# Kernel tuning notes

Measured on AMD Instinct MI355X. Metric: run time of the kernel, lower is better.

## Reference

```python
import jax, jax.numpy as jnp
import numpy as np

N_NODES = 2176
N_IN = 64
N_HID = 2048
N_OUT = 64
NODE_DIM = 64
HEADS = 4


def _build_edge_index():
    hs, os_ = N_IN, N_IN + N_HID
    # input -> hidden block (order: for i: for h)
    s1 = np.repeat(np.arange(0, N_IN), N_HID)
    t1 = np.tile(np.arange(hs, os_), N_IN)
    # hidden -> output block (order: for h: for o)
    s2 = np.repeat(np.arange(hs, os_), N_OUT)
    t2 = np.tile(np.arange(os_, N_NODES), N_HID)
    return jnp.asarray(np.stack([np.concatenate([s1, s2]), np.concatenate([t1, t2])]), dtype=jnp.int32)


def setup_inputs() -> dict:
    key = jax.random.key(0)
    ks = jax.random.split(key, 20)
    D, H = NODE_DIM, HEADS
    edge_index = _build_edge_index()  # [2, E]
    E = edge_index.shape[1]

    def xavier(k, shape):
        fan_in, fan_out = shape[0], shape[1]
        lim = float(np.sqrt(6.0 / (fan_in + fan_out)))
        return jax.random.uniform(k, shape, jnp.float32, -lim, lim)

    return {
        "x_input": jax.random.normal(ks[0], (N_IN,), jnp.float32),
        "node_features": jax.random.normal(ks[1], (N_NODES, D), jnp.float32) * 0.1,
        "edge_weights": jax.random.normal(ks[2], (E, 1), jnp.float32) * 0.1,
        "edge_index": edge_index,
        "wq1": xavier(ks[3], (D, D * H)), "wk1": xavier(ks[4], (D, D * H)),
        "wv1": xavier(ks[5], (D, D * H)), "we1": xavier(ks[6], (1, H)),
        "wo1": xavier(ks[7], (D * H, D)), "bo1": jnp.zeros((D,), jnp.float32),
        "wq2": xavier(ks[8], (D, D * H)), "wk2": xavier(ks[9], (D, D * H)),
        "wv2": xavier(ks[10], (D, D * H)), "we2": xavier(ks[11], (1, H)),
        "wo2": xavier(ks[12], (D * H, D)), "bo2": jnp.zeros((D,), jnp.float32),
        "wproj": xavier(ks[13], (D, 1)), "bproj": jnp.zeros((1,), jnp.float32),
        "num_output_nodes": N_OUT,
    }


def _message_pass(x, edge_index, ew, wq, wk, wv, we, wo, bo):
    # x: [N, D_in]; edge_index: [2, E]; ew: [E, 1]
    src, tgt = edge_index[0], edge_index[1]
    dout = wo.shape[1]
    heads = wq.shape[1] // dout
    q = (x[tgt] @ wq).reshape(-1, heads, dout)  # [E, H, D]
    k = (x[src] @ wk).reshape(-1, heads, dout)
    v = (x[src] @ wv).reshape(-1, heads, dout)
    attn = (q * k).sum(-1) / jnp.sqrt(jnp.float32(dout)) + ew @ we  # [E, H]
    # NOTE: the per-target segment-softmax in the torch source is dead code;
    # the effective math is leaky_relu then a global softmax over edges.
    attn = jax.nn.leaky_relu(attn, negative_slope=0.2)
    attn = jax.nn.softmax(attn, axis=0)
    weighted_v = (attn[:, :, None] * v).reshape(-1, heads * dout)  # [E, H*D]
    out = jax.ops.segment_sum(weighted_v, tgt, num_segments=x.shape[0])  # [N, H*D]
    out = out @ wo + bo
    return out + x  # residual (in_channels == out_channels)


def reference(x_input, node_features, edge_weights, edge_index,
              wq1, wk1, wv1, we1, wo1, bo1,
              wq2, wk2, wv2, we2, wo2, bo2,
              wproj, bproj, num_output_nodes):
    n_in = x_input.shape[0]
    x = node_features.at[:n_in, 0].set(x_input)
    x = jax.nn.relu(_message_pass(x, edge_index, edge_weights, wq1, wk1, wv1, we1, wo1, bo1))
    x = jax.nn.relu(_message_pass(x, edge_index, edge_weights, wq2, wk2, wv2, we2, wo2, bo2))
    out_nodes = x[x.shape[0] - num_output_nodes:]
    output = jax.nn.sigmoid(out_nodes @ wproj + bproj).squeeze()
    return output, x
```

## Files before the change

kernel.cpp:

```cpp
#include <hip/hip_runtime.h>
#include <math.h>

#define E1 131072

template<int AR, int K4>
__device__ __forceinline__ void gemm_nn(const float* __restrict__ A,
                                        const float* __restrict__ B,
                                        float acc[AR][4], int tr, int tc) {
  for (int k4 = 0; k4 < K4; ++k4) {
    float4 b0 = *(const float4*)&B[(k4 * 4 + 0) * 68 + tc * 4];
    float4 b1 = *(const float4*)&B[(k4 * 4 + 1) * 68 + tc * 4];
    float4 b2 = *(const float4*)&B[(k4 * 4 + 2) * 68 + tc * 4];
    float4 b3 = *(const float4*)&B[(k4 * 4 + 3) * 68 + tc * 4];
#pragma unroll
    for (int a = 0; a < AR; ++a) {
      float4 av = *(const float4*)&A[(tr + 16 * a) * 68 + k4 * 4];
      acc[a][0] += av.x * b0.x + av.y * b1.x + av.z * b2.x + av.w * b3.x;
      acc[a][1] += av.x * b0.y + av.y * b1.y + av.z * b2.y + av.w * b3.y;
      acc[a][2] += av.x * b0.z + av.y * b1.z + av.z * b2.z + av.w * b3.z;
      acc[a][3] += av.x * b0.w + av.y * b1.w + av.z * b2.w + av.w * b3.w;
    }
  }
}

template<int AR, int BR>
__device__ __forceinline__ void gemm_nt(const float* __restrict__ A,
                                        const float* __restrict__ B,
                                        float acc[AR][BR], int tr, int tc) {
  for (int k4 = 0; k4 < 16; ++k4) {
    float4 av[AR], bv[BR];
#pragma unroll
    for (int a = 0; a < AR; ++a) av[a] = *(const float4*)&A[(tr + 16 * a) * 68 + k4 * 4];
#pragma unroll
    for (int b = 0; b < BR; ++b) bv[b] = *(const float4*)&B[(tc + 16 * b) * 68 + k4 * 4];
#pragma unroll
    for (int a = 0; a < AR; ++a)
#pragma unroll
      for (int b = 0; b < BR; ++b)
        acc[a][b] += av[a].x * bv[b].x + av[a].y * bv[b].y +
                     av[a].z * bv[b].z + av[a].w * bv[b].w;
  }
}

template<int AR>
__device__ __forceinline__ void st_tile(float* __restrict__ C, const float acc[AR][4],
                                        int tr, int tc) {
#pragma unroll
  for (int a = 0; a < AR; ++a)
    *(float4*)&C[(tr + 16 * a) * 68 + tc * 4] =
        make_float4(acc[a][0], acc[a][1], acc[a][2], acc[a][3]);
}

__device__ __forceinline__ void ld64(float* __restrict__ dst, const float* __restrict__ src,
                                     int tid, bool sub, const float* __restrict__ xinp) {
  for (int t4 = tid; t4 < 1024; t4 += 256) {
    int r = t4 >> 4, c0 = (t4 & 15) * 4;
    float4 v = *(const float4*)(src + t4 * 4);
    if (sub && c0 == 0) v.x = xinp[r];
    *(float4*)&dst[r * 68 + c0] = v;
  }
}
__device__ __forceinline__ void ld32(float* __restrict__ dst, const float* __restrict__ src,
                                     int tid) {
  for (int t4 = tid; t4 < 512; t4 += 256) {
    int r = t4 >> 4, c0 = (t4 & 15) * 4;
    *(float4*)&dst[r * 68 + c0] = *(const float4*)(src + t4 * 4);
  }
}
__device__ __forceinline__ void ldw(float* __restrict__ dst, const float* __restrict__ w,
                                    int h, int tid) {
  for (int t4 = tid; t4 < 1024; t4 += 256) {
    int k = t4 >> 4, c0 = (t4 & 15) * 4;
    *(float4*)&dst[k * 68 + c0] = *(const float4*)(w + k * 256 + h * 64 + c0);
  }
}

__global__ __launch_bounds__(256) void k_pre(const float* __restrict__ nf,
                                             const float* __restrict__ xinp,
                                             const float* __restrict__ wq1, const float* __restrict__ wk1,
                                             const float* __restrict__ wv1, const float* __restrict__ wo1,
                                             const float* __restrict__ bo1,
                                             const float* __restrict__ wq2, const float* __restrict__ wk2,
                                             const float* __restrict__ wv2, const float* __restrict__ wo2,
                                             float* __restrict__ Y1b, float* __restrict__ Y2b,
                                             float* __restrict__ Y1pb, float* __restrict__ M2b,
                                             float* __restrict__ W2b) {
  __shared__ float A[4352];
  __shared__ float B[4352];
  __shared__ float C[4352];
  const int bid = blockIdx.x, tid = threadIdx.x;
  const int type = bid >> 2, h = bid & 3;
  const int tr = tid >> 4, tc = tid & 15;

  if (type <= 2) {
    if (type == 0) {
      ld64(A, nf, tid, true, xinp);
    } else if (type == 1) {
      ld64(A, nf + 2112 * 64, tid, false, nullptr);
    } else {
      for (int t4 = tid; t4 < 1024; t4 += 256) {
        int r = t4 >> 4, c0 = (t4 & 15) * 4;
        float4 v = *(const float4*)(nf + t4 * 4);
        if (c0 == 0) v.x = xinp[r];
        float4 bv = *(const float4*)(bo1 + c0);
        v.x = fmaxf(v.x + bv.x, 0.f); v.y = fmaxf(v.y + bv.y, 0.f);
        v.z = fmaxf(v.z + bv.z, 0.f); v.w = fmaxf(v.w + bv.w, 0.f);
        *(float4*)&A[r * 68 + c0] = v;
      }
    }
    const float* w1 = (type == 0) ? wk1 : (type == 1) ? wq1 : wk2;
    const float* w2 = (type == 0) ? wq1 : (type == 1) ? wk1 : wq2;
    ldw(B, w1, h, tid);
    __syncthreads();
    float t_[4][4];
#pragma unroll
    for (int a = 0; a < 4; ++a)
#pragma unroll
      for (int q = 0; q < 4; ++q) t_[a][q] = 0.f;
    gemm_nn<4, 16>(A, B, t_, tr, tc);
    __syncthreads();
    st_tile<4>(C, t_, tr, tc);
    ldw(B, w2, h, tid);
    __syncthreads();
    float y[4][4];
#pragma unroll
    for (int a = 0; a < 4; ++a)
#pragma unroll
      for (int b = 0; b < 4; ++b) y[a][b] = 0.f;
    gemm_nt<4, 4>(C, B, y, tr, tc);
    float* dst = (type == 0) ? Y1b : (type == 1) ? Y2b : Y1pb;
#pragma unroll
    for (int a = 0; a < 4; ++a)
#pragma unroll
      for (int b = 0; b < 4; ++b)
        dst[h * 4096 + (tr + 16 * a) * 64 + tc + 16 * b] = y[a][b];
  } else if (type == 3) {
    ldw(A, wq2, h, tid);
    ldw(B, wk2, h, tid);
    __syncthreads();
    float m[4][4];
#pragma unroll
    for (int a = 0; a < 4; ++a)
#pragma unroll
      for (int b = 0; b < 4; ++b) m[a][b] = 0.f;
    gemm_nt<4, 4>(A, B, m, tr, tc);
#pragma unroll
    for (int a = 0; a < 4; ++a)
#pragma unroll
      for (int b = 0; b < 4; ++b)
        M2b[h * 4096 + (tr + 16 * a) * 64 + tc + 16 * b] = m[a][b];
  } else {
    const float* wv = (type == 4) ? wv1 : wv2;
    const float* wo = (type == 4) ? wo1 : wo2;
    ldw(A, wv, h, tid);
    for (int t4 = tid; t4 < 1024; t4 += 256) {
      int t = t4 >> 4, c0 = (t4 & 15) * 4;
      *(float4*)&B[t * 68 + c0] = *(const float4*)(wo + (h * 64 + t) * 64 + c0);
    }
    __syncthreads();
    float m[4][4];
#pragma unroll
    for (int a = 0; a < 4; ++a)
#pragma unroll
      for (int q = 0; q < 4; ++q) m[a][q] = 0.f;
    gemm_nn<4, 16>(A, B, m, tr, tc);
    float* o = W2b + (type - 4) * 16384;
#pragma unroll
    for (int a = 0; a < 4; ++a)
      *(float4*)&o[(h * 64 + tr + 16 * a) * 64 + tc * 4] =
          make_float4(m[a][0], m[a][1], m[a][2], m[a][3]);
  }
}

__global__ __launch_bounds__(256) void k_attn1(const float* __restrict__ x,
                                               const float* __restrict__ xinp,
                                               const float* __restrict__ Y1b,
                                               const float* __restrict__ Y2b,
                                               const float* __restrict__ we,
                                               const float* __restrict__ ew,
                                               float* __restrict__ AggH,
                                               float* __restrict__ part,
                                               float* __restrict__ bsum) {
  __shared__ float S_[13184];
  __shared__ float wred[4];
  const int bid = blockIdx.x, tid = threadIdx.x;
  const int h = bid & 3;
  const int tr = tid >> 4, tc = tid & 15;
  const float weh = we[h];

  if (bid < 256) {
    const int j0 = (bid >> 2) * 32;
    float* XS = S_;
    float* Y  = S_ + 4352;
    float* XH = S_ + 8704;
    float* G  = S_ + 10880;
    ld64(XS, x, tid, true, xinp);
    ld64(Y, Y1b + h * 4096, tid, false, nullptr);
    ld32(XH, x + (64 + j0) * 64, tid);
    for (int t4 = tid; t4 < 512; t4 += 256) {
      int i = t4 >> 3, jl0 = (t4 & 7) * 4;
      *(float4*)&G[i * 36 + jl0] = *(const float4*)(ew + i * 2048 + j0 + jl0);
    }
    __syncthreads();
    float lg[2][4];
#pragma unroll
    for (int a = 0; a < 2; ++a)
#pragma unroll
      for (int b = 0; b < 4; ++b) lg[a][b] = 0.f;
    gemm_nt<2, 4>(XH, Y, lg, tr, tc);
    float e_[2][4], esum = 0.f;
#pragma unroll
    for (int a = 0; a < 2; ++a) {
      int row = tr + 16 * a;
#pragma unroll
      for (int b = 0; b < 4; ++b) {
        int col = tc + 16 * b;
        float v = lg[a][b] * 0.125f + G[col * 36 + row] * weh;
        v = (v >= 0.f) ? v : 0.2f * v;
        v = fminf(v, 60.f);
        float e = __expf(v);
        e_[a][b] = e; esum += e;
      }
    }
#pragma unroll
    for (int s = 1; s < 64; s <<= 1) esum += __shfl_xor(esum, s);
    if ((tid & 63) == 0) wred[tid >> 6] = esum;
    __syncthreads();
#pragma unroll
    for (int a = 0; a < 2; ++a)
#pragma unroll
      for (int b = 0; b < 4; ++b)
        XH[(tr + 16 * a) * 68 + tc + 16 * b] = e_[a][b];
    __syncthreads();
    float u[2][4];
#pragma unroll
    for (int a = 0; a < 2; ++a)
#pragma unroll
      for (int q = 0; q < 4; ++q) u[a][q] = 0.f;
    gemm_nn<2, 16>(XH, XS, u, tr, tc);
#pragma unroll
    for (int a = 0; a < 2; ++a)
      *(float4*)&AggH[(j0 + tr + 16 * a) * 256 + h * 64 + tc * 4] =
          make_float4(u[a][0], u[a][1], u[a][2], u[a][3]);
    if (tid == 0) bsum[bid] = (wred[0] + wred[1]) + (wred[2] + wred[3]);
  } else {
    const int tile = (bid - 256) >> 2;
    const int j0 = tile * 32;
    float* Y  = S_;
    float* XH = S_ + 4352;
    float* G  = S_ + 6528;
    ld64(Y, Y2b + h * 4096, tid, false, nullptr);
    ld32(XH, x + (64 + j0) * 64, tid);
    for (int t4 = tid; t4 < 512; t4 += 256) {
      int jl = t4 >> 4, o0 = (t4 & 15) * 4;
      *(float4*)&G[jl * 68 + o0] = *(const float4*)(ew + E1 + (j0 + jl) * 64 + o0);
    }
    __syncthreads();
    float lg[4][2];
#pragma unroll
    for (int a = 0; a < 4; ++a)
#pragma unroll
      for (int b = 0; b < 2; ++b) lg[a][b] = 0.f;
    gemm_nt<4, 2>(Y, XH, lg, tr, tc);
    float e_[4][2], esum = 0.f;
#pragma unroll
    for (int a = 0; a < 4; ++a) {
      int row = tr + 16 * a;
#pragma unroll
      for (int b = 0; b < 2; ++b) {
        int col = tc + 16 * b;
        float v = lg[a][b] * 0.125f + G[col * 68 + row] * weh;
        v = (v >= 0.f) ? v : 0.2f * v;
        v = fminf(v, 60.f);
        float e = __expf(v);
        e_[a][b] = e; esum += e;
      }
    }
#pragma unroll
    for (int s = 1; s < 64; s <<= 1) esum += __shfl_xor(esum, s);
    if ((tid & 63) == 0) wred[tid >> 6] = esum;
    __syncthreads();
#pragma unroll
    for (int a = 0; a < 4; ++a)
#pragma unroll
      for (int b = 0; b < 2; ++b)
        Y[(tr + 16 * a) * 68 + tc + 16 * b] = e_[a][b];
    __syncthreads();
    float u[4][4];
#pragma unroll
    for (int a = 0; a < 4; ++a)
#pragma unroll
      for (int q = 0; q < 4; ++q) u[a][q] = 0.f;
    gemm_nn<4, 8>(Y, XH, u, tr, tc);
#pragma unroll
    for (int a = 0; a < 4; ++a)
      *(float4*)&part[tile * 16384 + (tr + 16 * a) * 256 + h * 64 + tc * 4] =
          make_float4(u[a][0], u[a][1], u[a][2], u[a][3]);
    if (tid == 0) bsum[bid] = (wred[0] + wred[1]) + (wred[2] + wred[3]);
  }
}

__global__ __launch_bounds__(256) void k_attn2(const float* __restrict__ x,
                                               const float* __restrict__ Y1pb,
                                               const float* __restrict__ M2b,
                                               const float* __restrict__ we,
                                               const float* __restrict__ ew,
                                               float* __restrict__ AggH,
                                               float* __restrict__ part,
                                               float* __restrict__ bsum) {
  __shared__ float S_[13184];
  __shared__ float wred[4];
  const int bid = blockIdx.x, tid = threadIdx.x;
  const int h = bid & 3;
  const int tr = tid >> 4, tc = tid & 15;
  const float weh = we[h];

  if (bid < 256) {
    const int j0 = (bid >> 2) * 32;
    float* XS = S_;
    float* Y  = S_ + 4352;
    float* XH = S_ + 8704;
    float* G  = S_ + 10880;
    ld64(XS, x, tid, false, nullptr);
    ld64(Y, Y1pb + h * 4096, tid, false, nullptr);
    ld32(XH, x + (64 + j0) * 64, tid);
    for (int t4 = tid; t4 < 512; t4 += 256) {
      int i = t4 >> 3, jl0 = (t4 & 7) * 4;
      *(float4*)&G[i * 36 + jl0] = *(const float4*)(ew + i * 2048 + j0 + jl0);
    }
    __syncthreads();
    float lg[2][4];
#pragma unroll
    for (int a = 0; a < 2; ++a)
#pragma unroll
      for (int b = 0; b < 4; ++b) lg[a][b] = 0.f;
    gemm_nt<2, 4>(XH, Y, lg, tr, tc);
    float e_[2][4], esum = 0.f;
#pragma unroll
    for (int a = 0; a < 2; ++a) {
      int row = tr + 16 * a;
#pragma unroll
      for (int b = 0; b < 4; ++b) {
        int col = tc + 16 * b;
        float v = lg[a][b] * 0.125f + G[col * 36 + row] * weh;
        v = (v >= 0.f) ? v : 0.2f * v;
        v = fminf(v, 60.f);
        float e = __expf(v);
        e_[a][b] = e; esum += e;
      }
    }
#pragma unroll
    for (int s = 1; s < 64; s <<= 1) esum += __shfl_xor(esum, s);
    if ((tid & 63) == 0) wred[tid >> 6] = esum;
    __syncthreads();
#pragma unroll
    for (int a = 0; a < 2; ++a)
#pragma unroll
      for (int b = 0; b < 4; ++b)
        XH[(tr + 16 * a) * 68 + tc + 16 * b] = e_[a][b];
    __syncthreads();
    float u[2][4];
#pragma unroll
    for (int a = 0; a < 2; ++a)
#pragma unroll
      for (int q = 0; q < 4; ++q) u[a][q] = 0.f;
    gemm_nn<2, 16>(XH, XS, u, tr, tc);
#pragma unroll
    for (int a = 0; a < 2; ++a)
      *(float4*)&AggH[(j0 + tr + 16 * a) * 256 + h * 64 + tc * 4] =
          make_float4(u[a][0], u[a][1], u[a][2], u[a][3]);
    if (tid == 0) bsum[bid] = (wred[0] + wred[1]) + (wred[2] + wred[3]);
  } else {
    const int tile = (bid - 256) >> 2;
    const int j0 = tile * 32;
    float* XO = S_;
    float* M  = S_ + 4352;
    float* XH = S_ + 8704;
    float* G  = S_ + 10880;
    ld64(XO, x + 2112 * 64, tid, false, nullptr);
    ld64(M, M2b + h * 4096, tid, false, nullptr);
    ld32(XH, x + (64 + j0) * 64, tid);
    for (int t4 = tid; t4 < 512; t4 += 256) {
      int jl = t4 >> 4, o0 = (t4 & 15) * 4;
      *(float4*)&G[jl * 68 + o0] = *(const float4*)(ew + E1 + (j0 + jl) * 64 + o0);
    }
    __syncthreads();
    float t_[4][4];
#pragma unroll
    for (int a = 0; a < 4; ++a)
#pragma unroll
      for (int q = 0; q < 4; ++q) t_[a][q] = 0.f;
    gemm_nn<4, 16>(XO, M, t_, tr, tc);
    __syncthreads();
    st_tile<4>(XO, t_, tr, tc);
    __syncthreads();
    float lg[4][2];
#pragma unroll
    for (int a = 0; a < 4; ++a)
#pragma unroll
      for (int b = 0; b < 2; ++b) lg[a][b] = 0.f;
    gemm_nt<4, 2>(XO, XH, lg, tr, tc);
    float esum = 0.f;
#pragma unroll
    for (int a = 0; a < 4; ++a) {
      int row = tr + 16 * a;
#pragma unroll
      for (int b = 0; b < 2; ++b) {
        int col = tc + 16 * b;
        float v = lg[a][b] * 0.125f + G[col * 68 + row] * weh;
        v = (v >= 0.f) ? v : 0.2f * v;
        v = fminf(v, 60.f);
        float e = __expf(v);
        esum += e;
        M[row * 68 + col] = e;
      }
    }
#pragma unroll
    for (int s = 1; s < 64; s <<= 1) esum += __shfl_xor(esum, s);
    if ((tid & 63) == 0) wred[tid >> 6] = esum;
    __syncthreads();
    float u[4][4];
#pragma unroll
    for (int a = 0; a < 4; ++a)
#pragma unroll
      for (int q = 0; q < 4; ++q) u[a][q] = 0.f;
    gemm_nn<4, 8>(M, XH, u, tr, tc);
#pragma unroll
    for (int a = 0; a < 4; ++a)
      *(float4*)&part[tile * 16384 + (tr + 16 * a) * 256 + h * 64 + tc * 4] =
          make_float4(u[a][0], u[a][1], u[a][2], u[a][3]);
    if (tid == 0) bsum[bid] = (wred[0] + wred[1]) + (wred[2] + wred[3]);
  }
}

template<bool SUB, bool HEAD>
__global__ __launch_bounds__(256) void k_proj(const float* __restrict__ xin,
                                              const float* __restrict__ xinp,
                                              const float* __restrict__ AggH,
                                              const float* __restrict__ part,
                                              const float* __restrict__ bsum,
                                              const float* __restrict__ W2,
                                              const float* __restrict__ bo,
                                              const float* __restrict__ wproj,
                                              const float* __restrict__ bproj,
                                              float* __restrict__ xout,
                                              float* __restrict__ outh) {
  __shared__ float As[4][260];
  const int bid = blockIdx.x, tid = threadIdx.x;
  const int n0 = bid * 4;
  const int nl = tid >> 6, d = tid & 63;
  const int node = n0 + nl;

  float inv[4];
  {
    int l = tid & 63;
#pragma unroll
    for (int hh = 0; hh < 4; ++hh) {
      float s = bsum[4 * l + hh] + bsum[256 + 4 * l + hh];
#pragma unroll
      for (int st = 1; st < 64; st <<= 1) s += __shfl_xor(s, st);
      inv[hh] = 1.f / s;
    }
  }

  float xres = xin[node * 64 + d];
  if (SUB) {
    if (d == 0 && node < 64) xres = xinp[node];
  }

  float val;
  if (n0 < 64) {
    val = xres + bo[d];
  } else {
    if (n0 < 2112) {
      int a = tid >> 6, c0 = (tid & 63) * 4;
      float4 v = *(const float4*)&AggH[(n0 - 64 + a) * 256 + c0];
      float iv = inv[c0 >> 6];
      *(float4*)&As[a][c0] = make_float4(v.x * iv, v.y * iv, v.z * iv, v.w * iv);
    } else {
      int a = tid >> 6, c0 = (tid & 63) * 4;
      float4 s = make_float4(0.f, 0.f, 0.f, 0.f);
      for (int ch = 0; ch < 64; ++ch) {
        float4 v = *(const float4*)&part[ch * 16384 + (n0 - 2112 + a) * 256 + c0];
        s.x += v.x; s.y += v.y; s.z += v.z; s.w += v.w;
      }
      float iv = inv[c0 >> 6];
      *(float4*)&As[a][c0] = make_float4(s.x * iv, s.y * iv, s.z * iv, s.w * iv);
    }
    __syncthreads();
    float acc = xres + bo[d];
    for (int c4 = 0; c4 < 64; ++c4) {
      float4 a4 = *(const float4*)&As[nl][c4 * 4];
      acc += a4.x * W2[(c4 * 4 + 0) * 64 + d] + a4.y * W2[(c4 * 4 + 1) * 64 + d] +
             a4.z * W2[(c4 * 4 + 2) * 64 + d] + a4.w * W2[(c4 * 4 + 3) * 64 + d];
    }
    val = acc;
  }
  val = fmaxf(val, 0.f);
  xout[node * 64 + d] = val;

  if (HEAD) {
    if (n0 >= 2112) {
      float wv = val * wproj[d];
#pragma unroll
      for (int st = 1; st < 64; st <<= 1) wv += __shfl_xor(wv, st);
      if ((tid & 63) == 0) outh[node - 2112] = 1.f / (1.f + __expf(-(wv + bproj[0])));
    }
  }
}

extern "C" void kernel_launch(void* const* d_in, const int* in_sizes, int n_in,
                              void* d_out, int out_size, void* d_ws, size_t ws_size,
                              hipStream_t stream) {
  const float* x_input       = (const float*)d_in[0];
  const float* node_features = (const float*)d_in[1];
  const float* edge_weights  = (const float*)d_in[2];
  const float* wq1 = (const float*)d_in[4];
  const float* wk1 = (const float*)d_in[5];
  const float* wv1 = (const float*)d_in[6];
  const float* we1 = (const float*)d_in[7];
  const float* wo1 = (const float*)d_in[8];
  const float* bo1 = (const float*)d_in[9];
  const float* wq2 = (const float*)d_in[10];
  const float* wk2 = (const float*)d_in[11];
  const float* wv2 = (const float*)d_in[12];
  const float* we2 = (const float*)d_in[13];
  const float* wo2 = (const float*)d_in[14];
  const float* bo2 = (const float*)d_in[15];
  const float* wproj = (const float*)d_in[16];
  const float* bproj = (const float*)d_in[17];

  float* out = (float*)d_out;
  float* ws = (float*)d_ws;
  float* xB   = ws;
  float* AggH = xB + 139264;
  float* part = AggH + 524288;
  float* bsum = part + 1048576;
  float* Y1b  = bsum + 512;
  float* Y2b  = Y1b + 16384;
  float* Y1pb = Y2b + 16384;
  float* M2b  = Y1pb + 16384;
  float* W2b  = M2b + 16384;

  k_pre<<<24, 256, 0, stream>>>(node_features, x_input, wq1, wk1, wv1, wo1, bo1,
                                wq2, wk2, wv2, wo2, Y1b, Y2b, Y1pb, M2b, W2b);
  k_attn1<<<512, 256, 0, stream>>>(node_features, x_input, Y1b, Y2b, we1,
                                   edge_weights, AggH, part, bsum);
  k_proj<true, false><<<544, 256, 0, stream>>>(node_features, x_input, AggH, part, bsum,
                                               W2b, bo1, nullptr, nullptr, xB, nullptr);
  k_attn2<<<512, 256, 0, stream>>>(xB, Y1pb, M2b, we2, edge_weights, AggH, part, bsum);
  k_proj<false, true><<<544, 256, 0, stream>>>(xB, nullptr, AggH, part, bsum,
                                               W2b + 16384, bo2, wproj, bproj, out + 64, out);
}
```

Measured before the change: 63.01 us.

## Fuse weight-precompute kernel into layer-1 attention kernel

Result: no change. 63.94 us (+1.5%).

```diff
diff --git a/kernel.cpp b/kernel.cpp
--- a/kernel.cpp
+++ b/kernel.cpp
@@ -75,140 +75,73 @@
   }
 }
 
-__global__ __launch_bounds__(256) void k_pre(const float* __restrict__ nf,
-                                             const float* __restrict__ xinp,
-                                             const float* __restrict__ wq1, const float* __restrict__ wk1,
-                                             const float* __restrict__ wv1, const float* __restrict__ wo1,
-                                             const float* __restrict__ bo1,
-                                             const float* __restrict__ wq2, const float* __restrict__ wk2,
-                                             const float* __restrict__ wv2, const float* __restrict__ wo2,
-                                             float* __restrict__ Y1b, float* __restrict__ Y2b,
-                                             float* __restrict__ Y1pb, float* __restrict__ M2b,
-                                             float* __restrict__ W2b) {
-  __shared__ float A[4352];
-  __shared__ float B[4352];
-  __shared__ float C[4352];
-  const int bid = blockIdx.x, tid = threadIdx.x;
-  const int type = bid >> 2, h = bid & 3;
-  const int tr = tid >> 4, tc = tid & 15;
-
-  if (type <= 2) {
-    if (type == 0) {
-      ld64(A, nf, tid, true, xinp);
-    } else if (type == 1) {
-      ld64(A, nf + 2112 * 64, tid, false, nullptr);
-    } else {
-      for (int t4 = tid; t4 < 1024; t4 += 256) {
-        int r = t4 >> 4, c0 = (t4 & 15) * 4;
-        float4 v = *(const float4*)(nf + t4 * 4);
-        if (c0 == 0) v.x = xinp[r];
-        float4 bv = *(const float4*)(bo1 + c0);
-        v.x = fmaxf(v.x + bv.x, 0.f); v.y = fmaxf(v.y + bv.y, 0.f);
-        v.z = fmaxf(v.z + bv.z, 0.f); v.w = fmaxf(v.w + bv.w, 0.f);
-        *(float4*)&A[r * 68 + c0] = v;
-      }
-    }
-    const float* w1 = (type == 0) ? wk1 : (type == 1) ? wq1 : wk2;
-    const float* w2 = (type == 0) ? wq1 : (type == 1) ? wk1 : wq2;
-    ldw(B, w1, h, tid);
-    __syncthreads();
-    float t_[4][4];
-#pragma unroll
-    for (int a = 0; a < 4; ++a)
-#pragma unroll
-      for (int q = 0; q < 4; ++q) t_[a][q] = 0.f;
-    gemm_nn<4, 16>(A, B, t_, tr, tc);
-    __syncthreads();
-    st_tile<4>(C, t_, tr, tc);
-    ldw(B, w2, h, tid);
-    __syncthreads();
-    float y[4][4];
-#pragma unroll
-    for (int a = 0; a < 4; ++a)
-#pragma unroll
-      for (int b = 0; b < 4; ++b) y[a][b] = 0.f;
-    gemm_nt<4, 4>(C, B, y, tr, tc);
-    float* dst = (type == 0) ? Y1b : (type == 1) ? Y2b : Y1pb;
-#pragma unroll
-    for (int a = 0; a < 4; ++a)
-#pragma unroll
-      for (int b = 0; b < 4; ++b)
-        dst[h * 4096 + (tr + 16 * a) * 64 + tc + 16 * b] = y[a][b];
-  } else if (type == 3) {
-    ldw(A, wq2, h, tid);
-    ldw(B, wk2, h, tid);
-    __syncthreads();
-    float m[4][4];
-#pragma unroll
-    for (int a = 0; a < 4; ++a)
-#pragma unroll
-      for (int b = 0; b < 4; ++b) m[a][b] = 0.f;
-    gemm_nt<4, 4>(A, B, m, tr, tc);
-#pragma unroll
-    for (int a = 0; a < 4; ++a)
-#pragma unroll
-      for (int b = 0; b < 4; ++b)
-        M2b[h * 4096 + (tr + 16 * a) * 64 + tc + 16 * b] = m[a][b];
-  } else {
-    const float* wv = (type == 4) ? wv1 : wv2;
-    const float* wo = (type == 4) ? wo1 : wo2;
-    ldw(A, wv, h, tid);
-    for (int t4 = tid; t4 < 1024; t4 += 256) {
-      int t = t4 >> 4, c0 = (t4 & 15) * 4;
-      *(float4*)&B[t * 68 + c0] = *(const float4*)(wo + (h * 64 + t) * 64 + c0);
-    }
-    __syncthreads();
-    float m[4][4];
-#pragma unroll
-    for (int a = 0; a < 4; ++a)
-#pragma unroll
-      for (int q = 0; q < 4; ++q) m[a][q] = 0.f;
-    gemm_nn<4, 16>(A, B, m, tr, tc);
-    float* o = W2b + (type - 4) * 16384;
-#pragma unroll
-    for (int a = 0; a < 4; ++a)
-      *(float4*)&o[(h * 64 + tr + 16 * a) * 64 + tc * 4] =
-          make_float4(m[a][0], m[a][1], m[a][2], m[a][3]);
-  }
-}
-
 __global__ __launch_bounds__(256) void k_attn1(const float* __restrict__ x,
                                                const float* __restrict__ xinp,
-                                               const float* __restrict__ Y1b,
-                                               const float* __restrict__ Y2b,
-                                               const float* __restrict__ we,
+                                               const float* __restrict__ wq1,
+                                               const float* __restrict__ wk1,
+                                               const float* __restrict__ we1,
                                                const float* __restrict__ ew,
+                                               const float* __restrict__ wq2,
+                                               const float* __restrict__ wk2,
+                                               const float* __restrict__ wv1,
+                                               const float* __restrict__ wo1,
+                                               const float* __restrict__ wv2,
+                                               const float* __restrict__ wo2,
+                                               const float* __restrict__ bo1,
                                                float* __restrict__ AggH,
                                                float* __restrict__ part,
-                                               float* __restrict__ bsum) {
-  __shared__ float S_[13184];
+                                               float* __restrict__ bsum,
+                                               float* __restrict__ Y1pb,
+                                               float* __restrict__ M2b,
+                                               float* __restrict__ W2b) {
+  __shared__ float S_[19712];
   __shared__ float wred[4];
   const int bid = blockIdx.x, tid = threadIdx.x;
   const int h = bid & 3;
   const int tr = tid >> 4, tc = tid & 15;
-  const float weh = we[h];
+  const float weh = we1[h];
 
   if (bid < 256) {
     const int j0 = (bid >> 2) * 32;
     float* XS = S_;
-    float* Y  = S_ + 4352;
-    float* XH = S_ + 8704;
-    float* G  = S_ + 10880;
+    float* W  = S_ + 4352;
+    float* Kt = S_ + 8704;
+    float* XH = S_ + 13056;
+    float* Qt = S_ + 15232;
+    float* G  = S_ + 17408;
     ld64(XS, x, tid, true, xinp);
-    ld64(Y, Y1b + h * 4096, tid, false, nullptr);
     ld32(XH, x + (64 + j0) * 64, tid);
+    ldw(W, wk1, h, tid);
     for (int t4 = tid; t4 < 512; t4 += 256) {
       int i = t4 >> 3, jl0 = (t4 & 7) * 4;
       *(float4*)&G[i * 36 + jl0] = *(const float4*)(ew + i * 2048 + j0 + jl0);
     }
     __syncthreads();
+    float kt[4][4];
+#pragma unroll
+    for (int a = 0; a < 4; ++a)
+#pragma unroll
+      for (int q = 0; q < 4; ++q) kt[a][q] = 0.f;
+    gemm_nn<4, 16>(XS, W, kt, tr, tc);
+    __syncthreads();
+    st_tile<4>(Kt, kt, tr, tc);
+    ldw(W, wq1, h, tid);
+    __syncthreads();
+    float qt[2][4];
+#pragma unroll
+    for (int a = 0; a < 2; ++a)
+#pragma unroll
+      for (int q = 0; q < 4; ++q) qt[a][q] = 0.f;
+    gemm_nn<2, 16>(XH, W, qt, tr, tc);
+    st_tile<2>(Qt, qt, tr, tc);
+    __syncthreads();
     float lg[2][4];
 #pragma unroll
     for (int a = 0; a < 2; ++a)
 #pragma unroll
       for (int b = 0; b < 4; ++b) lg[a][b] = 0.f;
-    gemm_nt<2, 4>(XH, Y, lg, tr, tc);
-    float e_[2][4], esum = 0.f;
+    gemm_nt<2, 4>(Qt, Kt, lg, tr, tc);
+    float esum = 0.f;
 #pragma unroll
     for (int a = 0; a < 2; ++a) {
       int row = tr + 16 * a;
@@ -219,18 +152,13 @@
         v = (v >= 0.f) ? v : 0.2f * v;
         v = fminf(v, 60.f);
         float e = __expf(v);
-        e_[a][b] = e; esum += e;
+        esum += e;
+        XH[row * 68 + col] = e;
       }
     }
 #pragma unroll
     for (int s = 1; s < 64; s <<= 1) esum += __shfl_xor(esum, s);
     if ((tid & 63) == 0) wred[tid >> 6] = esum;
-    __syncthreads();
-#pragma unroll
-    for (int a = 0; a < 2; ++a)
-#pragma unroll
-      for (int b = 0; b < 4; ++b)
-        XH[(tr + 16 * a) * 68 + tc + 16 * b] = e_[a][b];
     __syncthreads();
     float u[2][4];
 #pragma unroll
@@ -243,25 +171,124 @@
       *(float4*)&AggH[(j0 + tr + 16 * a) * 256 + h * 64 + tc * 4] =
           make_float4(u[a][0], u[a][1], u[a][2], u[a][3]);
     if (tid == 0) bsum[bid] = (wred[0] + wred[1]) + (wred[2] + wred[3]);
+
+    if (bid < 16) {
+      __syncthreads();
+      const int type = bid >> 2, hh = bid & 3;
+      float* A = S_;
+      float* B = S_ + 4352;
+      float* C = S_ + 8704;
+      if (type == 0) {
+        for (int t4 = tid; t4 < 1024; t4 += 256) {
+          int r = t4 >> 4, c0 = (t4 & 15) * 4;
+          float4 v = *(const float4*)(x + t4 * 4);
+          if (c0 == 0) v.x = xinp[r];
+          float4 bv = *(const float4*)(bo1 + c0);
+          v.x = fmaxf(v.x + bv.x, 0.f); v.y = fmaxf(v.y + bv.y, 0.f);
+          v.z = fmaxf(v.z + bv.z, 0.f); v.w = fmaxf(v.w + bv.w, 0.f);
+          *(float4*)&A[r * 68 + c0] = v;
+        }
+        ldw(B, wk2, hh, tid);
+        __syncthreads();
+        float t_[4][4];
+#pragma unroll
+        for (int a = 0; a < 4; ++a)
+#pragma unroll
+          for (int q = 0; q < 4; ++q) t_[a][q] = 0.f;
+        gemm_nn<4, 16>(A, B, t_, tr, tc);
+        __syncthreads();
+        st_tile<4>(C, t_, tr, tc);
+        ldw(B, wq2, hh, tid);
+        __syncthreads();
+        float y[4][4];
+#pragma unroll
+        for (int a = 0; a < 4; ++a)
+#pragma unroll
+          for (int b = 0; b < 4; ++b) y[a][b] = 0.f;
+        gemm_nt<4, 4>(C, B, y, tr, tc);
+#pragma unroll
+        for (int a = 0; a < 4; ++a)
+#pragma unroll
+          for (int b = 0; b < 4; ++b)
+            Y1pb[hh * 4096 + (tr + 16 * a) * 64 + tc + 16 * b] = y[a][b];
+      } else if (type == 1) {
+        ldw(A, wq2, hh, tid);
+        ldw(B, wk2, hh, tid);
+        __syncthreads();
+        float m[4][4];
+#pragma unroll
+        for (int a = 0; a < 4; ++a)
+#pragma unroll
+          for (int b = 0; b < 4; ++b) m[a][b] = 0.f;
+        gemm_nt<4, 4>(A, B, m, tr, tc);
+#pragma unroll
+        for (int a = 0; a < 4; ++a)
+#pragma unroll
+          for (int b = 0; b < 4; ++b)
+            M2b[hh * 4096 + (tr + 16 * a) * 64 + tc + 16 * b] = m[a][b];
+      } else {
+        const float* wv = (type == 2) ? wv1 : wv2;
+        const float* wo = (type == 2) ? wo1 : wo2;
+        ldw(A, wv, hh, tid);
+        for (int t4 = tid; t4 < 1024; t4 += 256) {
+          int t = t4 >> 4, c0 = (t4 & 15) * 4;
+          *(float4*)&B[t * 68 + c0] = *(const float4*)(wo + (hh * 64 + t) * 64 + c0);
+        }
+        __syncthreads();
+        float m[4][4];
+#pragma unroll
+        for (int a = 0; a < 4; ++a)
+#pragma unroll
+          for (int q = 0; q < 4; ++q) m[a][q] = 0.f;
+        gemm_nn<4, 16>(A, B, m, tr, tc);
+        float* o = W2b + (type - 2) * 16384;
+#pragma unroll
+        for (int a = 0; a < 4; ++a)
+          *(float4*)&o[(hh * 64 + tr + 16 * a) * 64 + tc * 4] =
+              make_float4(m[a][0], m[a][1], m[a][2], m[a][3]);
+      }
+    }
   } else {
     const int tile = (bid - 256) >> 2;
     const int j0 = tile * 32;
-    float* Y  = S_;
-    float* XH = S_ + 4352;
-    float* G  = S_ + 6528;
-    ld64(Y, Y2b + h * 4096, tid, false, nullptr);
+    float* XO = S_;
+    float* W  = S_ + 4352;
+    float* Qt = S_ + 8704;
+    float* XH = S_ + 13056;
+    float* Kt = S_ + 15232;
+    float* G  = S_ + 17408;
+    ld64(XO, x + 2112 * 64, tid, false, nullptr);
     ld32(XH, x + (64 + j0) * 64, tid);
+    ldw(W, wk1, h, tid);
     for (int t4 = tid; t4 < 512; t4 += 256) {
       int jl = t4 >> 4, o0 = (t4 & 15) * 4;
       *(float4*)&G[jl * 68 + o0] = *(const float4*)(ew + E1 + (j0 + jl) * 64 + o0);
     }
     __syncthreads();
+    float kt[2][4];
+#pragma unroll
+    for (int a = 0; a < 2; ++a)
+#pragma unroll
+      for (int q = 0; q < 4; ++q) kt[a][q] = 0.f;
+    gemm_nn<2, 16>(XH, W, kt, tr, tc);
+    __syncthreads();
+    st_tile<2>(Kt, kt, tr, tc);
+    ldw(W, wq1, h, tid);
+    __syncthreads();
+    float qt[4][4];
+#pragma unroll
+    for (int a = 0; a < 4; ++a)
+#pragma unroll
+      for (int q = 0; q < 4; ++q) qt[a][q] = 0.f;
+    gemm_nn<4, 16>(XO, W, qt, tr, tc);
+    st_tile<4>(Qt, qt, tr, tc);
+    __syncthreads();
     float lg[4][2];
 #pragma unroll
     for (int a = 0; a < 4; ++a)
 #pragma unroll
       for (int b = 0; b < 2; ++b) lg[a][b] = 0.f;
-    gemm_nt<4, 2>(Y, XH, lg, tr, tc);
+    gemm_nt<4, 2>(Qt, Kt, lg, tr, tc);
     float e_[4][2], esum = 0.f;
 #pragma unroll
     for (int a = 0; a < 4; ++a) {
@@ -284,14 +311,14 @@
     for (int a = 0; a < 4; ++a)
 #pragma unroll
       for (int b = 0; b < 2; ++b)
-        Y[(tr + 16 * a) * 68 + tc + 16 * b] = e_[a][b];
+        Qt[(tr + 16 * a) * 68 + tc + 16 * b] = e_[a][b];
     __syncthreads();
     float u[4][4];
 #pragma unroll
     for (int a = 0; a < 4; ++a)
 #pragma unroll
       for (int q = 0; q < 4; ++q) u[a][q] = 0.f;
-    gemm_nn<4, 8>(Y, XH, u, tr, tc);
+    gemm_nn<4, 8>(Qt, XH, u, tr, tc);
 #pragma unroll
     for (int a = 0; a < 4; ++a)
       *(float4*)&part[tile * 16384 + (tr + 16 * a) * 256 + h * 64 + tc * 4] =
@@ -536,16 +563,13 @@
   float* AggH = xB + 139264;
   float* part = AggH + 524288;
   float* bsum = part + 1048576;
-  float* Y1b  = bsum + 512;
-  float* Y2b  = Y1b + 16384;
-  float* Y1pb = Y2b + 16384;
+  float* Y1pb = bsum + 512;
   float* M2b  = Y1pb + 16384;
   float* W2b  = M2b + 16384;
 
-  k_pre<<<24, 256, 0, stream>>>(node_features, x_input, wq1, wk1, wv1, wo1, bo1,
-                                wq2, wk2, wv2, wo2, Y1b, Y2b, Y1pb, M2b, W2b);
-  k_attn1<<<512, 256, 0, stream>>>(node_features, x_input, Y1b, Y2b, we1,
-                                   edge_weights, AggH, part, bsum);
+  k_attn1<<<512, 256, 0, stream>>>(node_features, x_input, wq1, wk1, we1, edge_weights,
+                                   wq2, wk2, wv1, wo1, wv2, wo2, bo1,
+                                   AggH, part, bsum, Y1pb, M2b, W2b);
   k_proj<true, false><<<544, 256, 0, stream>>>(node_features, x_input, AggH, part, bsum,
                                                W2b, bo1, nullptr, nullptr, xB, nullptr);
   k_attn2<<<512, 256, 0, stream>>>(xB, Y1pb, M2b, we2, edge_weights, AggH, part, bsum);
```
